# Optimization experiments

Hardware: AMD Instinct MI355X
Metric: run time of the kernel (lower is better)

## Reference

```python
import jax, jax.numpy as jnp
import numpy as np

N = 50000
E = 800000
D = 128
DOUT = 128
KEEP_SCALE = 2.0  # 1 / (1 - drop_rate), drop_rate = 0.5


def setup_inputs() -> dict:
    key = jax.random.key(0)
    k1, k2, k3, k4, k5, k6 = jax.random.split(key, 6)
    X = jax.random.normal(k1, (N, D), dtype=jnp.float32)
    W = jax.random.normal(k2, (2 * D, DOUT), dtype=jnp.float32) * (1.0 / np.sqrt(2 * D))
    b = jax.random.normal(k3, (DOUT,), dtype=jnp.float32) * 0.01
    src = jax.random.randint(k4, (E,), 0, N, dtype=jnp.int32)
    dst = jax.random.randint(k5, (E,), 0, N, dtype=jnp.int32)
    drop_mask = jax.random.randint(k6, (N, DOUT), 0, 2, dtype=jnp.int32)
    return {"X": X, "W": W, "b": b, "src": src, "dst": dst, "drop_mask": drop_mask}


def reference(X, W, b, src, dst, drop_mask):
    # v2v mean aggregation: X_nbr[i] = mean_{(j->i) in E} X[j]
    nbr_sum = jax.ops.segment_sum(X[src], dst, num_segments=N)        # [N, D]
    deg = jax.ops.segment_sum(jnp.ones((E,), X.dtype), dst, num_segments=N)  # [N]
    X_nbr = nbr_sum / jnp.maximum(deg, 1.0)[:, None]
    # concat + linear + relu + dropout (deterministic mask, train-mode scaling)
    H = jnp.concatenate([X, X_nbr], axis=1)                           # [N, 2D]
    out = jax.nn.relu(H @ W + b)
    out = out * (drop_mask.astype(out.dtype) * KEEP_SCALE)
    return out
```

## Files before the change

kernel.cpp:

```cpp
#include <hip/hip_runtime.h>

#define NN 50000
#define ND 50048
#define NW 6256
#define NE 800000
#define CHUNKS 32
#define EPC 25000
#define CAP 56
#define NTILE 3125
#define CVT_UNITS 1600000
#define CVT_BLOCKS 1563

typedef __attribute__((ext_vector_type(8))) short short8;
typedef __attribute__((ext_vector_type(4))) float f32x4;
typedef __attribute__((ext_vector_type(2))) float f32x2;
typedef __attribute__((ext_vector_type(4))) unsigned int u32x4;
typedef __attribute__((ext_vector_type(2))) unsigned int u32x2;


__device__ __forceinline__ unsigned f2bf(float f) {
  unsigned u = __builtin_bit_cast(unsigned, f);
  return (u + 0x7fffu + ((u >> 16) & 1u)) >> 16;
}

#if defined(__has_builtin) && __has_builtin(__builtin_amdgcn_cvt_pk_fp8_f32) && \
    __has_builtin(__builtin_amdgcn_cvt_pk_f32_fp8)
#define FP8_HW 1
#else
#define FP8_HW 0
#endif

#if !FP8_HW
__device__ __forceinline__ unsigned f2fp8(float x) {
  unsigned u = __builtin_bit_cast(unsigned, x);
  unsigned s = (u >> 24) & 0x80u;
  float a = __builtin_bit_cast(float, u & 0x7fffffffu);
  if (a < 0.015625f) {
    unsigned q = (unsigned)(a * 512.0f + 0.5f);
    return s | (q == 8u ? 0x08u : q);
  }
  if (a >= 448.0f) return s | 0x7Eu;
  unsigned v = u & 0x7fffffffu;
  v = v + 0x0007FFFFu + ((v >> 20) & 1u);
  unsigned e = (v >> 23) - 120u;
  if (e >= 16u) return s | 0x7Eu;
  return s | (e << 3) | ((v >> 20) & 7u);
}
__device__ __forceinline__ float fp82f(unsigned b) {
  unsigned s = (b & 0x80u) << 24;
  unsigned e = (b >> 3) & 15u;
  unsigned m = b & 7u;
  unsigned mag = e ? ((e + 120u) << 23) | (m << 20)
                   : __builtin_bit_cast(unsigned, (float)m * 0.001953125f);
  return __builtin_bit_cast(float, s | mag);
}
#endif

__global__ __launch_bounds__(1024) void k_rankconv(const int* __restrict__ dst,
                                                   const float* __restrict__ W,
                                                   const float* __restrict__ X,
                                                   unsigned char* __restrict__ rank,
                                                   unsigned int* __restrict__ chunkcnt,
                                                   u32x4* __restrict__ Wfrag,
                                                   u32x2* __restrict__ Xbf2,
                                                   unsigned int* __restrict__ Xf8w) {
  int tid = threadIdx.x;
  int c = blockIdx.x;
  if (c >= CHUNKS) {
    int i = (c - CHUNKS) * 1024 + tid;
    if (i < CVT_UNITS + 32) {
      f32x4 v = (f32x4){0.f, 0.f, 0.f, 0.f};
      if (i < CVT_UNITS) v = ((const f32x4*)X)[i];
      u32x2 o;
      o[0] = f2bf(v[0]) | (f2bf(v[1]) << 16);
      o[1] = f2bf(v[2]) | (f2bf(v[3]) << 16);
      Xbf2[i] = o;
      unsigned p8;
#if FP8_HW
      p8 = __builtin_amdgcn_cvt_pk_fp8_f32(v[0], v[1], 0, false);
      p8 = __builtin_amdgcn_cvt_pk_fp8_f32(v[2], v[3], p8, true);
#else
      p8 = f2fp8(v[0]) | (f2fp8(v[1]) << 8) | (f2fp8(v[2]) << 16) | (f2fp8(v[3]) << 24);
#endif
      Xf8w[i] = p8;
    }
    return;
  }
  __shared__ unsigned int pack[NW];
  if (tid < 128) {
    int s = c * 128 + tid;
    int lane = s & 63;
    int t = (s >> 6) & 7;
    int kb = s >> 9;
    int col = t * 16 + (lane & 15);
    int k0 = kb * 32 + (lane >> 4) * 8;
    u32x4 o;
#pragma unroll
    for (int p = 0; p < 4; ++p) {
      unsigned lo = f2bf(W[(k0 + 2 * p) * 128 + col]);
      unsigned hi = f2bf(W[(k0 + 2 * p + 1) * 128 + col]);
      o[p] = lo | (hi << 16);
    }
    Wfrag[s] = o;
  }
  for (int w = tid; w < NW; w += 1024) pack[w] = 0;
  __syncthreads();
  int ebase = c * EPC;
  for (int i = tid; i < EPC; i += 1024) {
    int e = ebase + i;
    int d = dst[e];
    unsigned sh = (unsigned)(d & 7) * 4u;
    unsigned old = atomicAdd(&pack[d >> 3], 1u << sh);
    rank[e] = (unsigned char)((old >> sh) & 15u);
  }
  __syncthreads();
  for (int w = tid; w < NW; w += 1024) chunkcnt[(size_t)c * NW + w] = pack[w];
}

__global__ __launch_bounds__(64) void k_base(const unsigned int* __restrict__ chunkcnt,
                                             unsigned char* __restrict__ chunkbase,
                                             unsigned int* __restrict__ deg) {
  int d = blockIdx.x * 64 + threadIdx.x;
  if (d >= NN) return;
  int w = d >> 3;
  unsigned sh = (unsigned)(d & 7) * 4u;
  unsigned cnts[CHUNKS];
#pragma unroll
  for (int c = 0; c < CHUNKS; ++c) cnts[c] = chunkcnt[(size_t)c * NW + w];
  unsigned run = 0;
#pragma unroll
  for (int c = 0; c < CHUNKS; ++c) {
    chunkbase[(size_t)c * ND + d] = (unsigned char)run;
    run += (cnts[c] >> sh) & 15u;
  }
  deg[d] = run;
}

__global__ __launch_bounds__(256) void k_place(const int* __restrict__ src,
                                               const int* __restrict__ dst,
                                               const unsigned char* __restrict__ rank,
                                               const unsigned char* __restrict__ chunkbase,
                                               unsigned short* __restrict__ slots) {
  int e = blockIdx.x * 256 + threadIdx.x;
  if (e >= NE) return;
  int c = e / EPC;
  int d = dst[e];
  int pos = (int)chunkbase[(size_t)c * ND + d] + (int)rank[e];
  if (pos < CAP) slots[d * CAP + pos] = (unsigned short)src[e];
}

__global__ __launch_bounds__(256) void k_gather(const unsigned short* __restrict__ Xf8u,
                                                const unsigned int* __restrict__ deg,
                                                const unsigned short* __restrict__ slots,
                                                unsigned int* __restrict__ Xnbr32) {
  int lane = threadIdx.x & 63;
  int node = blockIdx.x * 4 + (threadIdx.x >> 6);
  int dg = (int)deg[node];
  int m = min(dg, CAP);
  const unsigned short* sl = slots + node * CAP;
  int s_pre = sl[min(lane, CAP - 1)];
  float a0 = 0.f, a1 = 0.f;

  for (int e0 = 0; e0 < m; e0 += 8) {
    int cnt = m - e0;
    unsigned short v[8];
#pragma unroll
    for (int j = 0; j < 8; ++j) {
      int s_ = __shfl(s_pre, e0 + j, 64);
      s_ = (j < cnt) ? s_ : NN;
      v[j] = Xf8u[(size_t)s_ * 64 + lane];
    }
#pragma unroll
    for (int j = 0; j < 8; ++j) {
#if FP8_HW
      f32x2 p = __builtin_amdgcn_cvt_pk_f32_fp8((int)(unsigned)v[j], false);
      a0 += p[0];
      a1 += p[1];
#else
      unsigned b_ = v[j];
      a0 += fp82f(b_ & 255u);
      a1 += fp82f((b_ >> 8) & 255u);
#endif
    }
  }
  float inv = 1.0f / (float)max(dg, 1);
  Xnbr32[(size_t)node * 64 + lane] = f2bf(a0 * inv) | (f2bf(a1 * inv) << 16);
}

__global__ __launch_bounds__(512) void k_gemm(const unsigned short* __restrict__ Xbf,
                                              const unsigned short* __restrict__ Xnbr,
                                              const u32x4* __restrict__ Wfrag,
                                              const float* __restrict__ b,
                                              const int* __restrict__ mask,
                                              float* __restrict__ out) {
  int lane = threadIdx.x & 63;
  int wid = threadIdx.x >> 6;
  int tile = blockIdx.x * 8 + wid;
  if (tile >= NTILE) return;

  int row = tile * 16 + (lane & 15);
  const u32x4* a0 = (const u32x4*)(Xbf + (size_t)row * 128) + (lane >> 4);
  const u32x4* a1 = (const u32x4*)(Xnbr + (size_t)row * 128) + (lane >> 4);

  float bias[8];
#pragma unroll
  for (int t = 0; t < 8; ++t) bias[t] = b[t * 16 + (lane & 15)];

  f32x4 acc[8];
#pragma unroll
  for (int t = 0; t < 8; ++t) acc[t] = (f32x4){0.f, 0.f, 0.f, 0.f};

#pragma unroll
  for (int kb = 0; kb < 4; ++kb) {
    short8 a = __builtin_bit_cast(short8, a0[kb * 4]);
#pragma unroll
    for (int t = 0; t < 8; ++t) {
      short8 w = __builtin_bit_cast(short8, Wfrag[(kb * 8 + t) * 64 + lane]);
      acc[t] = __builtin_amdgcn_mfma_f32_16x16x32_bf16(a, w, acc[t], 0, 0, 0);
    }
  }
#pragma unroll
  for (int kb = 0; kb < 4; ++kb) {
    short8 a = __builtin_bit_cast(short8, a1[kb * 4]);
#pragma unroll
    for (int t = 0; t < 8; ++t) {
      short8 w = __builtin_bit_cast(short8, Wfrag[((kb + 4) * 8 + t) * 64 + lane]);
      acc[t] = __builtin_amdgcn_mfma_f32_16x16x32_bf16(a, w, acc[t], 0, 0, 0);
    }
  }

  int orow = tile * 16 + (lane >> 4) * 4;
  int ocol = lane & 15;
#pragma unroll
  for (int t = 0; t < 8; ++t) {
#pragma unroll
    for (int rg = 0; rg < 4; ++rg) {
      size_t idx = (size_t)(orow + rg) * 128 + t * 16 + ocol;
      float v = fmaxf(acc[t][rg] + bias[t], 0.f);
      int mk = mask[idx];
      out[idx] = v * (2.0f * (float)mk);
    }
  }
}

extern "C" void kernel_launch(void* const* d_in, const int* in_sizes, int n_in,
                              void* d_out, int out_size, void* d_ws, size_t ws_size,
                              hipStream_t stream) {
  (void)in_sizes; (void)n_in; (void)out_size; (void)ws_size;
  const float* X = (const float*)d_in[0];
  const float* W = (const float*)d_in[1];
  const float* b = (const float*)d_in[2];
  const int* src = (const int*)d_in[3];
  const int* dst = (const int*)d_in[4];
  const int* mask = (const int*)d_in[5];
  float* out = (float*)d_out;

  char* ws = (char*)d_ws;
  u32x4* Wfrag = (u32x4*)ws;
  unsigned int* deg = (unsigned int*)(ws + 65536);
  unsigned short* slots = (unsigned short*)(ws + 265728);
  unsigned int* Xf8w = (unsigned int*)(ws + 5865728);
  const unsigned short* Xf8u = (const unsigned short*)(ws + 5865728);
  u32x2* Xbf2 = (u32x2*)(ws + 12265984);
  const unsigned short* Xbf = (const unsigned short*)(ws + 12265984);
  unsigned int* Xnbr32 = (unsigned int*)(ws + 25066240);
  const unsigned short* Xnbr = (const unsigned short*)(ws + 25066240);
  unsigned char* rank = (unsigned char*)(ws + 25066240);
  unsigned int* chunkcnt = (unsigned int*)(ws + 25866240);
  unsigned char* chunkbase = (unsigned char*)(ws + 26667008);

  k_rankconv<<<CHUNKS + CVT_BLOCKS, 1024, 0, stream>>>(dst, W, X, rank, chunkcnt, Wfrag,
                                                       Xbf2, Xf8w);
  k_base<<<(NN + 63) / 64, 64, 0, stream>>>(chunkcnt, chunkbase, deg);
  k_place<<<(NE + 255) / 256, 256, 0, stream>>>(src, dst, rank, chunkbase, slots);
  k_gather<<<NN / 4, 256, 0, stream>>>(Xf8u, deg, slots, Xnbr32);
  k_gemm<<<(NTILE + 7) / 8, 512, 0, stream>>>(Xbf, Xnbr, Wfrag, b, mask, out);
}
```

Before: 74.69 us.

## Split fp8 feature table into two column planes and gather each plane separately

```diff
diff --git a/kernel.cpp b/kernel.cpp
--- a/kernel.cpp
+++ b/kernel.cpp
@@ -10,6 +10,8 @@
 #define NTILE 3125
 #define CVT_UNITS 1600000
 #define CVT_BLOCKS 1563
+#define PLANEB 3200064
+#define PLANE32 800016
 
 typedef __attribute__((ext_vector_type(8))) short short8;
 typedef __attribute__((ext_vector_type(4))) float f32x4;
@@ -82,7 +84,9 @@
 #else
       p8 = f2fp8(v[0]) | (f2fp8(v[1]) << 8) | (f2fp8(v[2]) << 16) | (f2fp8(v[3]) << 24);
 #endif
-      Xf8w[i] = p8;
+      int r = i >> 5;
+      int d0 = (i & 31) * 4;
+      Xf8w[(d0 >> 6) * PLANE32 + r * 16 + ((d0 & 63) >> 2)] = p8;
     }
     return;
   }
@@ -149,42 +153,39 @@
   if (pos < CAP) slots[d * CAP + pos] = (unsigned short)src[e];
 }
 
-__global__ __launch_bounds__(256) void k_gather(const unsigned short* __restrict__ Xf8u,
-                                                const unsigned int* __restrict__ deg,
-                                                const unsigned short* __restrict__ slots,
-                                                unsigned int* __restrict__ Xnbr32) {
+__global__ __launch_bounds__(256) void k_gatherp(const unsigned char* __restrict__ plane,
+                                                 const unsigned int* __restrict__ deg,
+                                                 const unsigned short* __restrict__ slots,
+                                                 unsigned short* __restrict__ XnbrHalf) {
   int lane = threadIdx.x & 63;
   int node = blockIdx.x * 4 + (threadIdx.x >> 6);
   int dg = (int)deg[node];
   int m = min(dg, CAP);
   const unsigned short* sl = slots + node * CAP;
   int s_pre = sl[min(lane, CAP - 1)];
-  float a0 = 0.f, a1 = 0.f;
+  float a = 0.f;
 
   for (int e0 = 0; e0 < m; e0 += 8) {
     int cnt = m - e0;
-    unsigned short v[8];
+    unsigned v[8];
 #pragma unroll
     for (int j = 0; j < 8; ++j) {
       int s_ = __shfl(s_pre, e0 + j, 64);
       s_ = (j < cnt) ? s_ : NN;
-      v[j] = Xf8u[(size_t)s_ * 64 + lane];
+      v[j] = plane[(size_t)s_ * 64 + lane];
     }
 #pragma unroll
     for (int j = 0; j < 8; ++j) {
 #if FP8_HW
-      f32x2 p = __builtin_amdgcn_cvt_pk_f32_fp8((int)(unsigned)v[j], false);
-      a0 += p[0];
-      a1 += p[1];
+      f32x2 p = __builtin_amdgcn_cvt_pk_f32_fp8((int)v[j], false);
+      a += p[0];
 #else
-      unsigned b_ = v[j];
-      a0 += fp82f(b_ & 255u);
-      a1 += fp82f((b_ >> 8) & 255u);
+      a += fp82f(v[j]);
 #endif
     }
   }
   float inv = 1.0f / (float)max(dg, 1);
-  Xnbr32[(size_t)node * 64 + lane] = f2bf(a0 * inv) | (f2bf(a1 * inv) << 16);
+  XnbrHalf[(size_t)node * 128 + lane] = (unsigned short)f2bf(a * inv);
 }
 
 __global__ __launch_bounds__(512) void k_gemm(const unsigned short* __restrict__ Xbf,
@@ -260,10 +261,10 @@
   unsigned int* deg = (unsigned int*)(ws + 65536);
   unsigned short* slots = (unsigned short*)(ws + 265728);
   unsigned int* Xf8w = (unsigned int*)(ws + 5865728);
-  const unsigned short* Xf8u = (const unsigned short*)(ws + 5865728);
+  const unsigned char* Xf8 = (const unsigned char*)(ws + 5865728);
   u32x2* Xbf2 = (u32x2*)(ws + 12265984);
   const unsigned short* Xbf = (const unsigned short*)(ws + 12265984);
-  unsigned int* Xnbr32 = (unsigned int*)(ws + 25066240);
+  unsigned short* XnbrW = (unsigned short*)(ws + 25066240);
   const unsigned short* Xnbr = (const unsigned short*)(ws + 25066240);
   unsigned char* rank = (unsigned char*)(ws + 25066240);
   unsigned int* chunkcnt = (unsigned int*)(ws + 25866240);
@@ -273,6 +274,7 @@
                                                        Xbf2, Xf8w);
   k_base<<<(NN + 63) / 64, 64, 0, stream>>>(chunkcnt, chunkbase, deg);
   k_place<<<(NE + 255) / 256, 256, 0, stream>>>(src, dst, rank, chunkbase, slots);
-  k_gather<<<NN / 4, 256, 0, stream>>>(Xf8u, deg, slots, Xnbr32);
+  k_gatherp<<<NN / 4, 256, 0, stream>>>(Xf8, deg, slots, XnbrW);
+  k_gatherp<<<NN / 4, 256, 0, stream>>>(Xf8 + PLANEB, deg, slots, XnbrW + 64);
   k_gemm<<<(NTILE + 7) / 8, 512, 0, stream>>>(Xbf, Xnbr, Wfrag, b, mask, out);
 }
```

Result: slower. 92.91 us (+24.4%).
